# Kernel optimization log

Measured on AMD Instinct MI355X. Metric: run time of the kernel, lower is better.

## Reference

```python
import jax, jax.numpy as jnp
import numpy as np

N_NODES = 10000
N_EDGES = 640000
NODE_DIM = 64
HIDDEN = 128
NUM_LAYERS = 4


def setup_inputs() -> dict:
    key = jax.random.key(0)
    ks = jax.random.split(key, 12)
    s = lambda fan_in: 1.0 / np.sqrt(fan_in)
    inp = {
        'x': jax.random.normal(ks[0], (N_NODES, NODE_DIM), dtype=jnp.float32),
        'edge_index': jax.random.randint(ks[1], (2, N_EDGES), 0, N_NODES, dtype=jnp.int64),
        # node embedding Linear(node_dim, hidden)
        'W_emb': jax.random.uniform(ks[2], (NODE_DIM, HIDDEN), jnp.float32, -s(NODE_DIM), s(NODE_DIM)),
        'b_emb': jnp.zeros((HIDDEN,), jnp.float32),
        # per-layer EdgeConv MLP: Linear(2*hidden, hidden) -> ReLU -> Linear(hidden, hidden)
        'W1': jax.random.uniform(ks[3], (NUM_LAYERS, 2 * HIDDEN, HIDDEN), jnp.float32, -s(2 * HIDDEN), s(2 * HIDDEN)),
        'b1': jnp.zeros((NUM_LAYERS, HIDDEN), jnp.float32),
        'W2': jax.random.uniform(ks[4], (NUM_LAYERS, HIDDEN, HIDDEN), jnp.float32, -s(HIDDEN), s(HIDDEN)),
        'b2': jnp.zeros((NUM_LAYERS, HIDDEN), jnp.float32),
        # final fc Linear(hidden, hidden)
        'W_fc': jax.random.uniform(ks[5], (HIDDEN, HIDDEN), jnp.float32, -s(HIDDEN), s(HIDDEN)),
        'b_fc': jnp.zeros((HIDDEN,), jnp.float32),
    }
    return inp


def _edge_conv(x, src, dst, W1, b1, W2, b2):
    # message: MLP(concat[x_i, x_j - x_i]); x_i = target (dst), x_j = source (src)
    x_i = x[dst]                      # [E, H]
    x_j = x[src]                      # [E, H]
    m = jnp.concatenate([x_i, x_j - x_i], axis=1)  # [E, 2H]
    m = jax.nn.relu(m @ W1 + b1)
    m = m @ W2 + b2                   # [E, H]
    # scatter-max aggregation at target nodes (self loops guarantee coverage)
    return jax.ops.segment_max(m, dst, num_segments=N_NODES)


def reference(x, edge_index, W_emb, b_emb, W1, b1, W2, b2, W_fc, b_fc):
    # add_self_loops
    loops = jnp.arange(N_NODES, dtype=edge_index.dtype)
    src = jnp.concatenate([edge_index[0], loops])
    dst = jnp.concatenate([edge_index[1], loops])

    h = x @ W_emb + b_emb             # [N, H]
    for l in range(NUM_LAYERS):
        h = _edge_conv(h, src, dst, W1[l], b1[l], W2[l], b2[l])
    return h @ W_fc + b_fc
```

## Files before the change

### kernel.cpp

```cpp
#include <hip/hip_runtime.h>

#define N_NODES 10000
#define N_EDGES 640000
#define NODE_DIM 64
#define HIDDEN 128
#define NUM_LAYERS 4
#define NT (N_EDGES + N_NODES)
#define EB8 64

typedef __attribute__((ext_vector_type(8))) short short8v;
typedef __attribute__((ext_vector_type(16))) float f32x16;

__global__ void k_init(const int* __restrict__ ei, int* __restrict__ flag,
                       int* __restrict__ cnt, unsigned int* __restrict__ enc0)
{
    int gid = blockIdx.x * 256 + threadIdx.x;
    if (gid < N_NODES) cnt[gid] = 0;
    for (int i = gid; i < N_NODES * HIDDEN; i += (int)gridDim.x * 256)
        enc0[i] = 0u;
    if (blockIdx.x == 0) {
        __shared__ int nz;
        if (threadIdx.x == 0) nz = 0;
        __syncthreads();
        int found = 0;
        for (int k = threadIdx.x; k < 2048; k += 256) {
            int pos = 2 * (k * 156) + 1;
            if (ei[pos] != 0) found = 1;
        }
        if (found) atomicOr(&nz, 1);
        __syncthreads();
        if (threadIdx.x == 0) flag[0] = nz;
    }
}

__global__ void k_norm_count(const int* __restrict__ ei, const int* __restrict__ flag,
                             int* __restrict__ srcN, int* __restrict__ dstN,
                             int* __restrict__ cnt)
{
    int e = blockIdx.x * 256 + threadIdx.x;
    if (e >= N_EDGES) return;
    int s, d;
    if (flag[0]) { s = ei[e];     d = ei[N_EDGES + e]; }
    else         { s = ei[2 * e]; d = ei[2 * (N_EDGES + e)]; }
    srcN[e] = s;
    dstN[e] = d;
    atomicAdd(&cnt[d], 1);
}

__global__ void k_scan(const int* __restrict__ cnt, int* __restrict__ cursor)
{
    __shared__ int part[256];
    const int t = threadIdx.x;
    const int CH = (N_NODES + 255) / 256;
    int lo = t * CH, hi = min(N_NODES, lo + CH);
    int s = 0;
    for (int i = lo; i < hi; ++i) s += cnt[i] + 1;
    part[t] = s;
    __syncthreads();
    for (int off = 1; off < 256; off <<= 1) {
        int v = (t >= off) ? part[t - off] : 0;
        __syncthreads();
        part[t] += v;
        __syncthreads();
    }
    int base = (t == 0) ? 0 : part[t - 1];
    for (int i = lo; i < hi; ++i) {
        cursor[i] = base;
        base += cnt[i] + 1;
    }
}

__global__ void k_scatter_all(const int* __restrict__ srcN, const int* __restrict__ dstN,
                              int* __restrict__ cursor,
                              int* __restrict__ esrc, int* __restrict__ edst)
{
    int e = blockIdx.x * 256 + threadIdx.x;
    if (e >= NT) return;
    int s, d;
    if (e < N_EDGES) { s = srcN[e]; d = dstN[e]; }
    else             { s = e - N_EDGES; d = s; }
    int pos = atomicAdd(&cursor[d], 1);
    esrc[pos] = s;
    edst[pos] = d;
}

__device__ __forceinline__ unsigned short bf16rne(float f)
{
    unsigned int u = __float_as_uint(f);
    unsigned int r = u + 0x7FFFu + ((u >> 16) & 1u);
    return (unsigned short)(r >> 16);
}

__global__ void k_prepww(const float* __restrict__ W1, const float* __restrict__ W2,
                         float* __restrict__ Wa, float* __restrict__ Wb,
                         short* __restrict__ W2f)
{
    int i = blockIdx.x * 256 + threadIdx.x;
    if (i >= NUM_LAYERS * 128 * 128) return;
    int l = i >> 14, rem = i & 16383;
    float top = W1[l * 32768 + rem];
    float bot = W1[l * 32768 + 16384 + rem];
    Wa[i] = top - bot;
    Wb[i] = bot;

    int k = rem >> 7, n = rem & 127;
    float w = W2[i];
    unsigned short hs = bf16rne(w);
    float hf = __uint_as_float((unsigned int)hs << 16);
    unsigned short ls = bf16rne(w - hf);
    int c = k >> 4, kh = (k >> 3) & 1, j = k & 7;
    int tile = n >> 5, m = n & 31;
    int lane = kh * 32 + m;
    size_t base = (size_t)l * 32768 + c * 4096 + tile * 1024 + lane * 8 + j;
    W2f[base]       = (short)hs;
    W2f[base + 512] = (short)ls;
}

__device__ __forceinline__ unsigned int encf(float f)
{
    unsigned int b = __float_as_uint(f);
    return b ^ ((unsigned int)((int)b >> 31) | 0x80000000u);
}

__device__ __forceinline__ float decenc(unsigned int u)
{
    unsigned int bits = (u & 0x80000000u) ? (u ^ 0x80000000u) : ~u;
    return __uint_as_float(bits);
}

__device__ __forceinline__ void radd_split4(float4 a, float4 b, uint2& H, uint2& L)
{
    float f0 = fmaxf(a.x + b.x, 0.f), f1 = fmaxf(a.y + b.y, 0.f);
    float f2 = fmaxf(a.z + b.z, 0.f), f3 = fmaxf(a.w + b.w, 0.f);
    unsigned int u0 = __float_as_uint(f0), u1 = __float_as_uint(f1);
    unsigned int u2 = __float_as_uint(f2), u3 = __float_as_uint(f3);
    H.x = (u1 & 0xFFFF0000u) | (u0 >> 16);
    H.y = (u3 & 0xFFFF0000u) | (u2 >> 16);
    float r0 = f0 - __uint_as_float(u0 & 0xFFFF0000u);
    float r1 = f1 - __uint_as_float(u1 & 0xFFFF0000u);
    float r2 = f2 - __uint_as_float(u2 & 0xFFFF0000u);
    float r3 = f3 - __uint_as_float(u3 & 0xFFFF0000u);
    L.x = (__float_as_uint(r0) >> 16) | (__float_as_uint(r1) & 0xFFFF0000u);
    L.y = (__float_as_uint(r2) >> 16) | (__float_as_uint(r3) & 0xFFFF0000u);
}

template <int K, bool HASB, bool DEC>
__global__ __launch_bounds__(256) void k_gemm64(
    const float* __restrict__ Xf, const unsigned int* __restrict__ enc,
    unsigned int* __restrict__ encZ, const float* __restrict__ bprev,
    const float* __restrict__ WA, const float* __restrict__ WB,
    const float* __restrict__ biasA,
    float* __restrict__ CA, float* __restrict__ CB, int M)
{
    constexpr int LDX = K + 4;
    __shared__ float Xs[64 * LDX];
    const int t = threadIdx.x;
    const int row0 = (blockIdx.x >> 1) * 64;
    const int ch   = (blockIdx.x & 1) * 64;
    constexpr int F4R = K / 4;
    for (int i = t; i < 64 * F4R; i += 256) {
        int r = i / F4R, f = i % F4R;
        int gr = row0 + r;
        float4 v = make_float4(0.f, 0.f, 0.f, 0.f);
        if (gr < M) {
            if constexpr (DEC) {
                uint4 u = *(const uint4*)(enc + (size_t)gr * K + 4 * f);
                v.x = decenc(u.x) + bprev[4 * f + 0];
                v.y = decenc(u.y) + bprev[4 * f + 1];
                v.z = decenc(u.z) + bprev[4 * f + 2];
                v.w = decenc(u.w) + bprev[4 * f + 3];
                if (encZ && ch == 0) {
                    uint4 z = make_uint4(0u, 0u, 0u, 0u);
                    *(uint4*)(encZ + (size_t)gr * K + 4 * f) = z;
                }
            } else {
                v = *(const float4*)(Xf + (size_t)gr * K + 4 * f);
            }
        }
        *(float4*)(Xs + r * LDX + 4 * f) = v;
    }
    __syncthreads();

    const int rg = t >> 4, cg = t & 15;
    {
        float accA[4][4];
#pragma unroll
        for (int i = 0; i < 4; ++i)
#pragma unroll
            for (int j = 0; j < 4; ++j) accA[i][j] = 0.f;
#pragma unroll 4
        for (int k = 0; k < K; ++k) {
            float4 wa = *(const float4*)(WA + k * 128 + ch + cg * 4);
            float xs[4];
#pragma unroll
            for (int i = 0; i < 4; ++i) xs[i] = Xs[(rg * 4 + i) * LDX + k];
#pragma unroll
            for (int i = 0; i < 4; ++i) {
                accA[i][0] += xs[i] * wa.x; accA[i][1] += xs[i] * wa.y;
                accA[i][2] += xs[i] * wa.z; accA[i][3] += xs[i] * wa.w;
            }
        }
        float4 b = *(const float4*)(biasA + ch + cg * 4);
#pragma unroll
        for (int i = 0; i < 4; ++i) {
            int r = row0 + rg * 4 + i;
            if (r < M) {
                *(float4*)(CA + (size_t)r * 128 + ch + cg * 4) =
                    make_float4(accA[i][0] + b.x, accA[i][1] + b.y,
                                accA[i][2] + b.z, accA[i][3] + b.w);
            }
        }
    }
    if constexpr (HASB) {
        float accB[4][4];
#pragma unroll
        for (int i = 0; i < 4; ++i)
#pragma unroll
            for (int j = 0; j < 4; ++j) accB[i][j] = 0.f;
#pragma unroll 4
        for (int k = 0; k < K; ++k) {
            float4 wb = *(const float4*)(WB + k * 128 + ch + cg * 4);
            float xs[4];
#pragma unroll
            for (int i = 0; i < 4; ++i) xs[i] = Xs[(rg * 4 + i) * LDX + k];
#pragma unroll
            for (int i = 0; i < 4; ++i) {
                accB[i][0] += xs[i] * wb.x; accB[i][1] += xs[i] * wb.y;
                accB[i][2] += xs[i] * wb.z; accB[i][3] += xs[i] * wb.w;
            }
        }
#pragma unroll
        for (int i = 0; i < 4; ++i) {
            int r = row0 + rg * 4 + i;
            if (r < M) {
                *(float4*)(CB + (size_t)r * 128 + ch + cg * 4) =
                    make_float4(accB[i][0], accB[i][1], accB[i][2], accB[i][3]);
            }
        }
    }
}

__global__ __launch_bounds__(256, 4) void k_edge9(
    const float* __restrict__ A, const float* __restrict__ Bm,
    const int* __restrict__ esrc, const int* __restrict__ edst,
    const short* __restrict__ W2l, unsigned int* __restrict__ enc)
{
    __shared__ __align__(16) short Ts[2048 * 8];
    __shared__ int dsts[EB8];

    const int t = threadIdx.x;
    const int lane = t & 63;
    const int wv   = t >> 6;
    const int nwg = (int)gridDim.x;
    const int orig = (int)blockIdx.x;
    const int xcd = orig & 7, idx = orig >> 3;
    const int qq = nwg >> 3, rr = nwg & 7;
    const int bid = (xcd < rr ? xcd * (qq + 1) : rr * (qq + 1) + (xcd - rr) * qq) + idx;
    const int s0 = bid * EB8;

    const short* Wp = W2l + (size_t)wv * 1024 + (size_t)lane * 8;
    short8v bfh[8], bfl[8];
#pragma unroll
    for (int c = 0; c < 8; ++c) {
        bfh[c] = *(const short8v*)(Wp + (size_t)c * 4096);
        bfl[c] = *(const short8v*)(Wp + (size_t)c * 4096 + 512);
    }

    {
        const int row = t >> 2;
        const int q   = t & 3;
        const int slot = s0 + row;
        int dst = -1, src = 0;
        if (slot < NT) { dst = edst[slot]; src = esrc[slot]; }
        if (q == 0) dsts[row] = dst;
        const int sfrag = row >> 5;
        const int mrow  = row & 31;
        const int kh    = q >> 1;
        const int half  = q & 1;
        const int lbase = kh * 32 + mrow;

        if (dst >= 0) {
            const float* Ar = A  + (size_t)dst * HIDDEN + q * 4;
            const float* Br = Bm + (size_t)src * HIDDEN + q * 4;
#pragma unroll
            for (int r = 0; r < 8; ++r) {
                float4 av = *(const float4*)(Ar + r * 16);
                float4 bv = *(const float4*)(Br + r * 16);
                uint2 H, L;
                radd_split4(av, bv, H, L);
                const int c  = r;
                const int ih = ((sfrag)     * 8 + c) * 64 + lbase;
                const int il = ((2 + sfrag) * 8 + c) * 64 + lbase;
                *(uint2*)(&Ts[(size_t)(ih ^ c) * 8 + half * 4]) = H;
                *(uint2*)(&Ts[(size_t)(il ^ c) * 8 + half * 4]) = L;
            }
        } else {
            uint2 z = make_uint2(0u, 0u);
#pragma unroll
            for (int r = 0; r < 8; ++r) {
                const int c  = r;
                const int ih = ((sfrag)     * 8 + c) * 64 + lbase;
                const int il = ((2 + sfrag) * 8 + c) * 64 + lbase;
                *(uint2*)(&Ts[(size_t)(ih ^ c) * 8 + half * 4]) = z;
                *(uint2*)(&Ts[(size_t)(il ^ c) * 8 + half * 4]) = z;
            }
        }
    }
    __syncthreads();

    f32x16 acc0 = {0,0,0,0,0,0,0,0,0,0,0,0,0,0,0,0};
    f32x16 acc1 = {0,0,0,0,0,0,0,0,0,0,0,0,0,0,0,0};

#pragma unroll
    for (int c = 0; c < 8; ++c) {
        short8v ah0 = *(const short8v*)(&Ts[(size_t)(((0 * 8 + c) * 64 + lane) ^ c) * 8]);
        short8v ah1 = *(const short8v*)(&Ts[(size_t)(((1 * 8 + c) * 64 + lane) ^ c) * 8]);
        short8v al0 = *(const short8v*)(&Ts[(size_t)(((2 * 8 + c) * 64 + lane) ^ c) * 8]);
        short8v al1 = *(const short8v*)(&Ts[(size_t)(((3 * 8 + c) * 64 + lane) ^ c) * 8]);
        acc0 = __builtin_amdgcn_mfma_f32_32x32x16_bf16(ah0, bfh[c], acc0, 0, 0, 0);
        acc0 = __builtin_amdgcn_mfma_f32_32x32x16_bf16(al0, bfh[c], acc0, 0, 0, 0);
        acc0 = __builtin_amdgcn_mfma_f32_32x32x16_bf16(ah0, bfl[c], acc0, 0, 0, 0);
        acc1 = __builtin_amdgcn_mfma_f32_32x32x16_bf16(ah1, bfh[c], acc1, 0, 0, 0);
        acc1 = __builtin_amdgcn_mfma_f32_32x32x16_bf16(al1, bfh[c], acc1, 0, 0, 0);
        acc1 = __builtin_amdgcn_mfma_f32_32x32x16_bf16(ah1, bfl[c], acc1, 0, 0, 0);
    }

    const int m   = lane & 31;
    const int kh  = lane >> 5;
    const int col = wv * 32 + m;
    const int d_first = dsts[0];
    const int d_last  = dsts[EB8 - 1];
    if (d_first == d_last) {
        if (d_first >= 0) {
            float mx = fmaxf(acc0[0], acc1[0]);
#pragma unroll
            for (int r = 1; r < 16; ++r)
                mx = fmaxf(mx, fmaxf(acc0[r], acc1[r]));
            atomicMax(&enc[(size_t)d_first * HIDDEN + col], encf(mx));
        }
    } else {
        {
            float run = -3.4e38f;
            int curd = dsts[4 * kh];
#pragma unroll
            for (int r = 0; r < 16; ++r) {
                const int er = (r & 3) + 8 * (r >> 2) + 4 * kh;
                int d = dsts[er];
                if (d != curd) {
                    if (curd >= 0)
                        atomicMax(&enc[(size_t)curd * HIDDEN + col], encf(run));
                    curd = d;
                    run = -3.4e38f;
                }
                run = fmaxf(run, acc0[r]);
            }
            if (curd >= 0)
                atomicMax(&enc[(size_t)curd * HIDDEN + col], encf(run));
        }
        {
            float run = -3.4e38f;
            int curd = dsts[32 + 4 * kh];
#pragma unroll
            for (int r = 0; r < 16; ++r) {
                const int er = 32 + (r & 3) + 8 * (r >> 2) + 4 * kh;
                int d = dsts[er];
                if (d != curd) {
                    if (curd >= 0)
                        atomicMax(&enc[(size_t)curd * HIDDEN + col], encf(run));
                    curd = d;
                    run = -3.4e38f;
                }
                run = fmaxf(run, acc1[r]);
            }
            if (curd >= 0)
                atomicMax(&enc[(size_t)curd * HIDDEN + col], encf(run));
        }
    }
}

extern "C" void kernel_launch(void* const* d_in, const int* in_sizes, int n_in,
                              void* d_out, int out_size, void* d_ws, size_t ws_size,
                              hipStream_t stream)
{
    const float* x     = (const float*)d_in[0];
    const int*   ei    = (const int*)d_in[1];
    const float* W_emb = (const float*)d_in[2];
    const float* b_emb = (const float*)d_in[3];
    const float* W1    = (const float*)d_in[4];
    const float* b1    = (const float*)d_in[5];
    const float* W2    = (const float*)d_in[6];
    const float* b2    = (const float*)d_in[7];
    const float* W_fc  = (const float*)d_in[8];
    const float* b_fc  = (const float*)d_in[9];
    float* out = (float*)d_out;

    char* p = (char*)d_ws;
    auto alloc = [&](size_t bytes) {
        char* r = p;
        p += (bytes + 255) & ~(size_t)255;
        return r;
    };
    float* h    = (float*)alloc((size_t)N_NODES * HIDDEN * 4);
    float* Ab   = (float*)alloc((size_t)N_NODES * HIDDEN * 4);
    float* Bb   = (float*)alloc((size_t)N_NODES * HIDDEN * 4);
    unsigned int* enc0 = (unsigned int*)alloc((size_t)N_NODES * HIDDEN * 4);
    unsigned int* enc1 = (unsigned int*)alloc((size_t)N_NODES * HIDDEN * 4);
    float* Wa   = (float*)alloc((size_t)NUM_LAYERS * 16384 * 4);
    float* Wb   = (float*)alloc((size_t)NUM_LAYERS * 16384 * 4);
    short* W2f  = (short*)alloc((size_t)NUM_LAYERS * 32768 * 2);
    int* cursor = (int*)alloc(N_NODES * 4);
    int* cnt    = (int*)alloc(N_NODES * 4);
    int* esrc   = (int*)alloc((size_t)NT * 4);
    int* edst   = (int*)alloc((size_t)NT * 4);
    int* srcN   = (int*)alloc((size_t)N_EDGES * 4);
    int* dstN   = (int*)alloc((size_t)N_EDGES * 4);
    int* flag   = (int*)alloc(4);

    unsigned int* encs[2] = {enc0, enc1};

    const int EBLK = (N_EDGES + 255) / 256;
    const int GB   = 2 * ((N_NODES + 63) / 64);
    const int EG   = (NT + EB8 - 1) / EB8;

    k_init<<<(N_NODES * HIDDEN + 255) / 256, 256, 0, stream>>>(ei, flag, cnt, enc0);
    k_norm_count<<<EBLK, 256, 0, stream>>>(ei, flag, srcN, dstN, cnt);
    k_scan<<<1, 256, 0, stream>>>(cnt, cursor);
    k_scatter_all<<<(NT + 255) / 256, 256, 0, stream>>>(srcN, dstN, cursor, esrc, edst);
    k_prepww<<<(NUM_LAYERS * 16384 + 255) / 256, 256, 0, stream>>>(W1, W2, Wa, Wb, W2f);

    k_gemm64<NODE_DIM, false, false><<<GB, 256, 0, stream>>>(
        x, nullptr, nullptr, nullptr, W_emb, nullptr, b_emb, h, nullptr, N_NODES);

    for (int l = 0; l < NUM_LAYERS; ++l) {
        if (l == 0) {
            k_gemm64<HIDDEN, true, false><<<GB, 256, 0, stream>>>(
                h, nullptr, nullptr, nullptr, Wa, Wb, b1, Ab, Bb, N_NODES);
        } else {
            k_gemm64<HIDDEN, true, true><<<GB, 256, 0, stream>>>(
                nullptr, encs[(l - 1) & 1], encs[l & 1], b2 + (l - 1) * 128,
                Wa + l * 16384, Wb + l * 16384, b1 + l * 128, Ab, Bb, N_NODES);
        }
        k_edge9<<<EG, 256, 0, stream>>>(Ab, Bb, esrc, edst,
                                        W2f + (size_t)l * 32768, encs[l & 1]);
    }
    k_gemm64<HIDDEN, false, true><<<GB, 256, 0, stream>>>(
        nullptr, encs[(NUM_LAYERS - 1) & 1], nullptr, b2 + 3 * 128,
        W_fc, nullptr, b_fc, out, nullptr, N_NODES);
}
```

Baseline: 561.6 us.

## Halve edge tile to 32 edges per block and stream W2 fragments for occupancy

```diff
diff --git a/kernel.cpp b/kernel.cpp
--- a/kernel.cpp
+++ b/kernel.cpp
@@ -6,7 +6,7 @@
 #define HIDDEN 128
 #define NUM_LAYERS 4
 #define NT (N_EDGES + N_NODES)
-#define EB8 64
+#define EB10 32
 
 typedef __attribute__((ext_vector_type(8))) short short8v;
 typedef __attribute__((ext_vector_type(16))) float f32x16;
@@ -240,13 +240,13 @@
     }
 }
 
-__global__ __launch_bounds__(256, 4) void k_edge9(
+__global__ __launch_bounds__(256, 8) void k_edge10(
     const float* __restrict__ A, const float* __restrict__ Bm,
     const int* __restrict__ esrc, const int* __restrict__ edst,
     const short* __restrict__ W2l, unsigned int* __restrict__ enc)
 {
-    __shared__ __align__(16) short Ts[2048 * 8];
-    __shared__ int dsts[EB8];
+    __shared__ __align__(16) short Ts[1024 * 8];
+    __shared__ int dsts[EB10];
 
     const int t = threadIdx.x;
     const int lane = t & 63;
@@ -256,125 +256,105 @@
     const int xcd = orig & 7, idx = orig >> 3;
     const int qq = nwg >> 3, rr = nwg & 7;
     const int bid = (xcd < rr ? xcd * (qq + 1) : rr * (qq + 1) + (xcd - rr) * qq) + idx;
-    const int s0 = bid * EB8;
-
-    const short* Wp = W2l + (size_t)wv * 1024 + (size_t)lane * 8;
-    short8v bfh[8], bfl[8];
-#pragma unroll
-    for (int c = 0; c < 8; ++c) {
-        bfh[c] = *(const short8v*)(Wp + (size_t)c * 4096);
-        bfl[c] = *(const short8v*)(Wp + (size_t)c * 4096 + 512);
-    }
+    const int s0 = bid * EB10;
 
     {
-        const int row = t >> 2;
-        const int q   = t & 3;
+        const int row = t >> 3;
+        const int c   = t & 7;
         const int slot = s0 + row;
         int dst = -1, src = 0;
         if (slot < NT) { dst = edst[slot]; src = esrc[slot]; }
-        if (q == 0) dsts[row] = dst;
-        const int sfrag = row >> 5;
-        const int mrow  = row & 31;
-        const int kh    = q >> 1;
-        const int half  = q & 1;
-        const int lbase = kh * 32 + mrow;
+        if (c == 0) dsts[row] = dst;
+
+        const int u_h0 = (((0 + c) * 64 +      row) ^ c) * 8;
+        const int u_h1 = (((0 + c) * 64 + 32 + row) ^ c) * 8;
+        const int u_l0 = (((8 + c) * 64 +      row) ^ c) * 8;
+        const int u_l1 = (((8 + c) * 64 + 32 + row) ^ c) * 8;
 
         if (dst >= 0) {
-            const float* Ar = A  + (size_t)dst * HIDDEN + q * 4;
-            const float* Br = Bm + (size_t)src * HIDDEN + q * 4;
-#pragma unroll
-            for (int r = 0; r < 8; ++r) {
-                float4 av = *(const float4*)(Ar + r * 16);
-                float4 bv = *(const float4*)(Br + r * 16);
-                uint2 H, L;
-                radd_split4(av, bv, H, L);
-                const int c  = r;
-                const int ih = ((sfrag)     * 8 + c) * 64 + lbase;
-                const int il = ((2 + sfrag) * 8 + c) * 64 + lbase;
-                *(uint2*)(&Ts[(size_t)(ih ^ c) * 8 + half * 4]) = H;
-                *(uint2*)(&Ts[(size_t)(il ^ c) * 8 + half * 4]) = L;
-            }
+            const float* Ar = A  + (size_t)dst * HIDDEN + c * 16;
+            const float* Br = Bm + (size_t)src * HIDDEN + c * 16;
+            float4 a0 = *(const float4*)(Ar + 0);
+            float4 a1 = *(const float4*)(Ar + 4);
+            float4 a2 = *(const float4*)(Ar + 8);
+            float4 a3 = *(const float4*)(Ar + 12);
+            float4 b0 = *(const float4*)(Br + 0);
+            float4 b1 = *(const float4*)(Br + 4);
+            float4 b2 = *(const float4*)(Br + 8);
+            float4 b3 = *(const float4*)(Br + 12);
+            uint2 Ha, La, Hb, Lb;
+            radd_split4(a0, b0, Ha, La);
+            radd_split4(a1, b1, Hb, Lb);
+            uint4 H0 = make_uint4(Ha.x, Ha.y, Hb.x, Hb.y);
+            uint4 L0 = make_uint4(La.x, La.y, Lb.x, Lb.y);
+            radd_split4(a2, b2, Ha, La);
+            radd_split4(a3, b3, Hb, Lb);
+            uint4 H1 = make_uint4(Ha.x, Ha.y, Hb.x, Hb.y);
+            uint4 L1 = make_uint4(La.x, La.y, Lb.x, Lb.y);
+            *(uint4*)(&Ts[u_h0]) = H0;
+            *(uint4*)(&Ts[u_h1]) = H1;
+            *(uint4*)(&Ts[u_l0]) = L0;
+            *(uint4*)(&Ts[u_l1]) = L1;
         } else {
-            uint2 z = make_uint2(0u, 0u);
-#pragma unroll
-            for (int r = 0; r < 8; ++r) {
-                const int c  = r;
-                const int ih = ((sfrag)     * 8 + c) * 64 + lbase;
-                const int il = ((2 + sfrag) * 8 + c) * 64 + lbase;
-                *(uint2*)(&Ts[(size_t)(ih ^ c) * 8 + half * 4]) = z;
-                *(uint2*)(&Ts[(size_t)(il ^ c) * 8 + half * 4]) = z;
-            }
+            uint4 z = make_uint4(0u, 0u, 0u, 0u);
+            *(uint4*)(&Ts[u_h0]) = z;
+            *(uint4*)(&Ts[u_h1]) = z;
+            *(uint4*)(&Ts[u_l0]) = z;
+            *(uint4*)(&Ts[u_l1]) = z;
         }
     }
     __syncthreads();
 
-    f32x16 acc0 = {0,0,0,0,0,0,0,0,0,0,0,0,0,0,0,0};
-    f32x16 acc1 = {0,0,0,0,0,0,0,0,0,0,0,0,0,0,0,0};
+    f32x16 acc = {0,0,0,0,0,0,0,0,0,0,0,0,0,0,0,0};
+
+    const short* Wp = W2l + (size_t)wv * 1024 + (size_t)lane * 8;
+    short8v bh = *(const short8v*)(Wp);
+    short8v bl = *(const short8v*)(Wp + 512);
 
 #pragma unroll
     for (int c = 0; c < 8; ++c) {
-        short8v ah0 = *(const short8v*)(&Ts[(size_t)(((0 * 8 + c) * 64 + lane) ^ c) * 8]);
-        short8v ah1 = *(const short8v*)(&Ts[(size_t)(((1 * 8 + c) * 64 + lane) ^ c) * 8]);
-        short8v al0 = *(const short8v*)(&Ts[(size_t)(((2 * 8 + c) * 64 + lane) ^ c) * 8]);
-        short8v al1 = *(const short8v*)(&Ts[(size_t)(((3 * 8 + c) * 64 + lane) ^ c) * 8]);
-        acc0 = __builtin_amdgcn_mfma_f32_32x32x16_bf16(ah0, bfh[c], acc0, 0, 0, 0);
-        acc0 = __builtin_amdgcn_mfma_f32_32x32x16_bf16(al0, bfh[c], acc0, 0, 0, 0);
-        acc0 = __builtin_amdgcn_mfma_f32_32x32x16_bf16(ah0, bfl[c], acc0, 0, 0, 0);
-        acc1 = __builtin_amdgcn_mfma_f32_32x32x16_bf16(ah1, bfh[c], acc1, 0, 0, 0);
-        acc1 = __builtin_amdgcn_mfma_f32_32x32x16_bf16(al1, bfh[c], acc1, 0, 0, 0);
-        acc1 = __builtin_amdgcn_mfma_f32_32x32x16_bf16(ah1, bfl[c], acc1, 0, 0, 0);
+        short8v nbh, nbl;
+        if (c < 7) {
+            nbh = *(const short8v*)(Wp + (size_t)(c + 1) * 4096);
+            nbl = *(const short8v*)(Wp + (size_t)(c + 1) * 4096 + 512);
+        }
+        short8v ah = *(const short8v*)(&Ts[(size_t)((( c     ) * 64 + lane) ^ c) * 8]);
+        short8v al = *(const short8v*)(&Ts[(size_t)(((8 + c ) * 64 + lane) ^ c) * 8]);
+        acc = __builtin_amdgcn_mfma_f32_32x32x16_bf16(ah, bh, acc, 0, 0, 0);
+        acc = __builtin_amdgcn_mfma_f32_32x32x16_bf16(al, bh, acc, 0, 0, 0);
+        acc = __builtin_amdgcn_mfma_f32_32x32x16_bf16(ah, bl, acc, 0, 0, 0);
+        if (c < 7) { bh = nbh; bl = nbl; }
     }
 
     const int m   = lane & 31;
     const int kh  = lane >> 5;
     const int col = wv * 32 + m;
     const int d_first = dsts[0];
-    const int d_last  = dsts[EB8 - 1];
+    const int d_last  = dsts[EB10 - 1];
     if (d_first == d_last) {
         if (d_first >= 0) {
-            float mx = fmaxf(acc0[0], acc1[0]);
-#pragma unroll
-            for (int r = 1; r < 16; ++r)
-                mx = fmaxf(mx, fmaxf(acc0[r], acc1[r]));
+            float mx = acc[0];
+#pragma unroll
+            for (int r = 1; r < 16; ++r) mx = fmaxf(mx, acc[r]);
             atomicMax(&enc[(size_t)d_first * HIDDEN + col], encf(mx));
         }
     } else {
-        {
-            float run = -3.4e38f;
-            int curd = dsts[4 * kh];
-#pragma unroll
-            for (int r = 0; r < 16; ++r) {
-                const int er = (r & 3) + 8 * (r >> 2) + 4 * kh;
-                int d = dsts[er];
-                if (d != curd) {
-                    if (curd >= 0)
-                        atomicMax(&enc[(size_t)curd * HIDDEN + col], encf(run));
-                    curd = d;
-                    run = -3.4e38f;
-                }
-                run = fmaxf(run, acc0[r]);
-            }
-            if (curd >= 0)
-                atomicMax(&enc[(size_t)curd * HIDDEN + col], encf(run));
-        }
-        {
-            float run = -3.4e38f;
-            int curd = dsts[32 + 4 * kh];
-#pragma unroll
-            for (int r = 0; r < 16; ++r) {
-                const int er = 32 + (r & 3) + 8 * (r >> 2) + 4 * kh;
-                int d = dsts[er];
-                if (d != curd) {
-                    if (curd >= 0)
-                        atomicMax(&enc[(size_t)curd * HIDDEN + col], encf(run));
-                    curd = d;
-                    run = -3.4e38f;
-                }
-                run = fmaxf(run, acc1[r]);
-            }
-            if (curd >= 0)
-                atomicMax(&enc[(size_t)curd * HIDDEN + col], encf(run));
-        }
+        float run = -3.4e38f;
+        int curd = dsts[4 * kh];
+#pragma unroll
+        for (int r = 0; r < 16; ++r) {
+            const int er = (r & 3) + 8 * (r >> 2) + 4 * kh;
+            int d = dsts[er];
+            if (d != curd) {
+                if (curd >= 0)
+                    atomicMax(&enc[(size_t)curd * HIDDEN + col], encf(run));
+                curd = d;
+                run = -3.4e38f;
+            }
+            run = fmaxf(run, acc[r]);
+        }
+        if (curd >= 0)
+            atomicMax(&enc[(size_t)curd * HIDDEN + col], encf(run));
     }
 }
 
@@ -420,7 +400,7 @@
 
     const int EBLK = (N_EDGES + 255) / 256;
     const int GB   = 2 * ((N_NODES + 63) / 64);
-    const int EG   = (NT + EB8 - 1) / EB8;
+    const int EG   = (NT + EB10 - 1) / EB10;
 
     k_init<<<(N_NODES * HIDDEN + 255) / 256, 256, 0, stream>>>(ei, flag, cnt, enc0);
     k_norm_count<<<EBLK, 256, 0, stream>>>(ei, flag, srcN, dstN, cnt);
@@ -440,8 +420,8 @@
                 nullptr, encs[(l - 1) & 1], encs[l & 1], b2 + (l - 1) * 128,
                 Wa + l * 16384, Wb + l * 16384, b1 + l * 128, Ab, Bb, N_NODES);
         }
-        k_edge9<<<EG, 256, 0, stream>>>(Ab, Bb, esrc, edst,
-                                        W2f + (size_t)l * 32768, encs[l & 1]);
+        k_edge10<<<EG, 256, 0, stream>>>(Ab, Bb, esrc, edst,
+                                         W2f + (size_t)l * 32768, encs[l & 1]);
     }
     k_gemm64<HIDDEN, false, true><<<GB, 256, 0, stream>>>(
         nullptr, encs[(NUM_LAYERS - 1) & 1], nullptr, b2 + 3 * 128,
```

After: 638.8 us. +13.8%, slower.

## Move node GEMMs to split-bf16 MFMA with pre-swizzled weight fragments

Applied to the files above, without the earlier changes.

```diff
diff --git a/kernel.cpp b/kernel.cpp
--- a/kernel.cpp
+++ b/kernel.cpp
@@ -91,29 +91,41 @@
     return (unsigned short)(r >> 16);
 }
 
-__global__ void k_prepww(const float* __restrict__ W1, const float* __restrict__ W2,
-                         float* __restrict__ Wa, float* __restrict__ Wb,
-                         short* __restrict__ W2f)
-{
-    int i = blockIdx.x * 256 + threadIdx.x;
-    if (i >= NUM_LAYERS * 128 * 128) return;
-    int l = i >> 14, rem = i & 16383;
-    float top = W1[l * 32768 + rem];
-    float bot = W1[l * 32768 + 16384 + rem];
-    Wa[i] = top - bot;
-    Wb[i] = bot;
-
-    int k = rem >> 7, n = rem & 127;
-    float w = W2[i];
+__device__ __forceinline__ void wfrag_store(short* __restrict__ Wf, int k, int n, float w)
+{
     unsigned short hs = bf16rne(w);
     float hf = __uint_as_float((unsigned int)hs << 16);
     unsigned short ls = bf16rne(w - hf);
     int c = k >> 4, kh = (k >> 3) & 1, j = k & 7;
     int tile = n >> 5, m = n & 31;
     int lane = kh * 32 + m;
-    size_t base = (size_t)l * 32768 + c * 4096 + tile * 1024 + lane * 8 + j;
-    W2f[base]       = (short)hs;
-    W2f[base + 512] = (short)ls;
+    size_t base = (size_t)c * 4096 + tile * 1024 + lane * 8 + j;
+    Wf[base]       = (short)hs;
+    Wf[base + 512] = (short)ls;
+}
+
+__global__ void k_prepall(const float* __restrict__ W1, const float* __restrict__ W2,
+                          const float* __restrict__ W_emb, const float* __restrict__ W_fc,
+                          short* __restrict__ Waf, short* __restrict__ Wbf,
+                          short* __restrict__ W2f, short* __restrict__ Wembf,
+                          short* __restrict__ Wfcf)
+{
+    int i = blockIdx.x * 256 + threadIdx.x;
+    if (i < NUM_LAYERS * 16384) {
+        int l = i >> 14, rem = i & 16383;
+        int k = rem >> 7, n = rem & 127;
+        float top = W1[l * 32768 + rem];
+        float bot = W1[l * 32768 + 16384 + rem];
+        wfrag_store(Waf + (size_t)l * 32768, k, n, top - bot);
+        wfrag_store(Wbf + (size_t)l * 32768, k, n, bot);
+        wfrag_store(W2f + (size_t)l * 32768, k, n, W2[i]);
+    } else if (i < NUM_LAYERS * 16384 + 8192) {
+        int j = i - NUM_LAYERS * 16384;
+        wfrag_store(Wembf, j >> 7, j & 127, W_emb[j]);
+    } else if (i < NUM_LAYERS * 16384 + 8192 + 16384) {
+        int j = i - NUM_LAYERS * 16384 - 8192;
+        wfrag_store(Wfcf, j >> 7, j & 127, W_fc[j]);
+    }
 }
 
 __device__ __forceinline__ unsigned int encf(float f)
@@ -144,98 +156,119 @@
     L.y = (__float_as_uint(r2) >> 16) | (__float_as_uint(r3) & 0xFFFF0000u);
 }
 
+__device__ __forceinline__ void split4_rne(float4 f, uint2& H, uint2& L)
+{
+    unsigned int h0 = bf16rne(f.x), h1 = bf16rne(f.y);
+    unsigned int h2 = bf16rne(f.z), h3 = bf16rne(f.w);
+    H.x = h0 | (h1 << 16);
+    H.y = h2 | (h3 << 16);
+    float r0 = f.x - __uint_as_float(h0 << 16);
+    float r1 = f.y - __uint_as_float(h1 << 16);
+    float r2 = f.z - __uint_as_float(h2 << 16);
+    float r3 = f.w - __uint_as_float(h3 << 16);
+    unsigned int l0 = bf16rne(r0), l1 = bf16rne(r1);
+    unsigned int l2 = bf16rne(r2), l3 = bf16rne(r3);
+    L.x = l0 | (l1 << 16);
+    L.y = l2 | (l3 << 16);
+}
+
 template <int K, bool HASB, bool DEC>
-__global__ __launch_bounds__(256) void k_gemm64(
-    const float* __restrict__ Xf, const unsigned int* __restrict__ enc,
+__global__ __launch_bounds__(256) void k_gemmf(
+    const float* __restrict__ Xf, const unsigned int* __restrict__ encR,
     unsigned int* __restrict__ encZ, const float* __restrict__ bprev,
-    const float* __restrict__ WA, const float* __restrict__ WB,
+    const short* __restrict__ WAf, const short* __restrict__ WBf,
     const float* __restrict__ biasA,
     float* __restrict__ CA, float* __restrict__ CB, int M)
 {
-    constexpr int LDX = K + 4;
-    __shared__ float Xs[64 * LDX];
+    constexpr int CH = K / 16;
+    __shared__ __align__(16) short Ts[4 * CH * 64 * 8];
     const int t = threadIdx.x;
-    const int row0 = (blockIdx.x >> 1) * 64;
-    const int ch   = (blockIdx.x & 1) * 64;
-    constexpr int F4R = K / 4;
-    for (int i = t; i < 64 * F4R; i += 256) {
-        int r = i / F4R, f = i % F4R;
-        int gr = row0 + r;
-        float4 v = make_float4(0.f, 0.f, 0.f, 0.f);
-        if (gr < M) {
-            if constexpr (DEC) {
-                uint4 u = *(const uint4*)(enc + (size_t)gr * K + 4 * f);
-                v.x = decenc(u.x) + bprev[4 * f + 0];
-                v.y = decenc(u.y) + bprev[4 * f + 1];
-                v.z = decenc(u.z) + bprev[4 * f + 2];
-                v.w = decenc(u.w) + bprev[4 * f + 3];
-                if (encZ && ch == 0) {
-                    uint4 z = make_uint4(0u, 0u, 0u, 0u);
-                    *(uint4*)(encZ + (size_t)gr * K + 4 * f) = z;
+    const int row0 = blockIdx.x * 64;
+
+    {
+        const int row = t >> 2, q = t & 3;
+        const int gr = row0 + row;
+        const int sfrag = row >> 5, mrow = row & 31;
+        const int kh = q >> 1, half = q & 1;
+        const int lbase = kh * 32 + mrow;
+#pragma unroll
+        for (int r = 0; r < CH; ++r) {
+            float4 v = make_float4(0.f, 0.f, 0.f, 0.f);
+            if (gr < M) {
+                const int ko = q * 4 + r * 16;
+                if constexpr (DEC) {
+                    uint4 u = *(const uint4*)(encR + (size_t)gr * K + ko);
+                    v.x = decenc(u.x) + bprev[ko + 0];
+                    v.y = decenc(u.y) + bprev[ko + 1];
+                    v.z = decenc(u.z) + bprev[ko + 2];
+                    v.w = decenc(u.w) + bprev[ko + 3];
+                    if (encZ)
+                        *(uint4*)(encZ + (size_t)gr * K + ko) = make_uint4(0u, 0u, 0u, 0u);
+                } else {
+                    v = *(const float4*)(Xf + (size_t)gr * K + ko);
                 }
-            } else {
-                v = *(const float4*)(Xf + (size_t)gr * K + 4 * f);
             }
-        }
-        *(float4*)(Xs + r * LDX + 4 * f) = v;
+            uint2 H, L;
+            split4_rne(v, H, L);
+            const int c  = r;
+            const int ih = ((0 * 2 + sfrag) * CH + c) * 64 + lbase;
+            const int il = ((1 * 2 + sfrag) * CH + c) * 64 + lbase;
+            *(uint2*)(&Ts[(size_t)(ih ^ c) * 8 + half * 4]) = H;
+            *(uint2*)(&Ts[(size_t)(il ^ c) * 8 + half * 4]) = L;
+        }
     }
     __syncthreads();
 
-    const int rg = t >> 4, cg = t & 15;
-    {
-        float accA[4][4];
-#pragma unroll
-        for (int i = 0; i < 4; ++i)
-#pragma unroll
-            for (int j = 0; j < 4; ++j) accA[i][j] = 0.f;
-#pragma unroll 4
-        for (int k = 0; k < K; ++k) {
-            float4 wa = *(const float4*)(WA + k * 128 + ch + cg * 4);
-            float xs[4];
-#pragma unroll
-            for (int i = 0; i < 4; ++i) xs[i] = Xs[(rg * 4 + i) * LDX + k];
-#pragma unroll
-            for (int i = 0; i < 4; ++i) {
-                accA[i][0] += xs[i] * wa.x; accA[i][1] += xs[i] * wa.y;
-                accA[i][2] += xs[i] * wa.z; accA[i][3] += xs[i] * wa.w;
-            }
-        }
-        float4 b = *(const float4*)(biasA + ch + cg * 4);
-#pragma unroll
-        for (int i = 0; i < 4; ++i) {
-            int r = row0 + rg * 4 + i;
-            if (r < M) {
-                *(float4*)(CA + (size_t)r * 128 + ch + cg * 4) =
-                    make_float4(accA[i][0] + b.x, accA[i][1] + b.y,
-                                accA[i][2] + b.z, accA[i][3] + b.w);
-            }
-        }
-    }
-    if constexpr (HASB) {
-        float accB[4][4];
-#pragma unroll
-        for (int i = 0; i < 4; ++i)
-#pragma unroll
-            for (int j = 0; j < 4; ++j) accB[i][j] = 0.f;
-#pragma unroll 4
-        for (int k = 0; k < K; ++k) {
-            float4 wb = *(const float4*)(WB + k * 128 + ch + cg * 4);
-            float xs[4];
-#pragma unroll
-            for (int i = 0; i < 4; ++i) xs[i] = Xs[(rg * 4 + i) * LDX + k];
-#pragma unroll
-            for (int i = 0; i < 4; ++i) {
-                accB[i][0] += xs[i] * wb.x; accB[i][1] += xs[i] * wb.y;
-                accB[i][2] += xs[i] * wb.z; accB[i][3] += xs[i] * wb.w;
-            }
-        }
-#pragma unroll
-        for (int i = 0; i < 4; ++i) {
-            int r = row0 + rg * 4 + i;
-            if (r < M) {
-                *(float4*)(CB + (size_t)r * 128 + ch + cg * 4) =
-                    make_float4(accB[i][0], accB[i][1], accB[i][2], accB[i][3]);
-            }
+    const int lane = t & 63;
+    const int wv   = t >> 6;
+    f32x16 aA0 = {0,0,0,0,0,0,0,0,0,0,0,0,0,0,0,0};
+    f32x16 aA1 = {0,0,0,0,0,0,0,0,0,0,0,0,0,0,0,0};
+    f32x16 aB0 = {0,0,0,0,0,0,0,0,0,0,0,0,0,0,0,0};
+    f32x16 aB1 = {0,0,0,0,0,0,0,0,0,0,0,0,0,0,0,0};
+
+    const short* WpA = WAf + (size_t)wv * 1024 + (size_t)lane * 8;
+    const short* WpB = HASB ? (WBf + (size_t)wv * 1024 + (size_t)lane * 8) : nullptr;
+
+#pragma unroll
+    for (int c = 0; c < CH; ++c) {
+        short8v wah = *(const short8v*)(WpA + (size_t)c * 4096);
+        short8v wal = *(const short8v*)(WpA + (size_t)c * 4096 + 512);
+        short8v ah0 = *(const short8v*)(&Ts[(size_t)((((0 * 2 + 0) * CH + c) * 64 + lane) ^ c) * 8]);
+        short8v ah1 = *(const short8v*)(&Ts[(size_t)((((0 * 2 + 1) * CH + c) * 64 + lane) ^ c) * 8]);
+        short8v al0 = *(const short8v*)(&Ts[(size_t)((((1 * 2 + 0) * CH + c) * 64 + lane) ^ c) * 8]);
+        short8v al1 = *(const short8v*)(&Ts[(size_t)((((1 * 2 + 1) * CH + c) * 64 + lane) ^ c) * 8]);
+        aA0 = __builtin_amdgcn_mfma_f32_32x32x16_bf16(ah0, wah, aA0, 0, 0, 0);
+        aA0 = __builtin_amdgcn_mfma_f32_32x32x16_bf16(al0, wah, aA0, 0, 0, 0);
+        aA0 = __builtin_amdgcn_mfma_f32_32x32x16_bf16(ah0, wal, aA0, 0, 0, 0);
+        aA1 = __builtin_amdgcn_mfma_f32_32x32x16_bf16(ah1, wah, aA1, 0, 0, 0);
+        aA1 = __builtin_amdgcn_mfma_f32_32x32x16_bf16(al1, wah, aA1, 0, 0, 0);
+        aA1 = __builtin_amdgcn_mfma_f32_32x32x16_bf16(ah1, wal, aA1, 0, 0, 0);
+        if constexpr (HASB) {
+            short8v wbh = *(const short8v*)(WpB + (size_t)c * 4096);
+            short8v wbl = *(const short8v*)(WpB + (size_t)c * 4096 + 512);
+            aB0 = __builtin_amdgcn_mfma_f32_32x32x16_bf16(ah0, wbh, aB0, 0, 0, 0);
+            aB0 = __builtin_amdgcn_mfma_f32_32x32x16_bf16(al0, wbh, aB0, 0, 0, 0);
+            aB0 = __builtin_amdgcn_mfma_f32_32x32x16_bf16(ah0, wbl, aB0, 0, 0, 0);
+            aB1 = __builtin_amdgcn_mfma_f32_32x32x16_bf16(ah1, wbh, aB1, 0, 0, 0);
+            aB1 = __builtin_amdgcn_mfma_f32_32x32x16_bf16(al1, wbh, aB1, 0, 0, 0);
+            aB1 = __builtin_amdgcn_mfma_f32_32x32x16_bf16(ah1, wbl, aB1, 0, 0, 0);
+        }
+    }
+
+    const int m   = lane & 31;
+    const int kh  = lane >> 5;
+    const int col = wv * 32 + m;
+    const float bA = biasA[col];
+#pragma unroll
+    for (int r = 0; r < 16; ++r) {
+        const int er = (r & 3) + 8 * (r >> 2) + 4 * kh;
+        const int r0 = row0 + er;
+        const int r1 = row0 + 32 + er;
+        if (r0 < M) CA[(size_t)r0 * 128 + col] = aA0[r] + bA;
+        if (r1 < M) CA[(size_t)r1 * 128 + col] = aA1[r] + bA;
+        if constexpr (HASB) {
+            if (r0 < M) CB[(size_t)r0 * 128 + col] = aB0[r];
+            if (r1 < M) CB[(size_t)r1 * 128 + col] = aB1[r];
         }
     }
 }
@@ -405,9 +438,11 @@
     float* Bb   = (float*)alloc((size_t)N_NODES * HIDDEN * 4);
     unsigned int* enc0 = (unsigned int*)alloc((size_t)N_NODES * HIDDEN * 4);
     unsigned int* enc1 = (unsigned int*)alloc((size_t)N_NODES * HIDDEN * 4);
-    float* Wa   = (float*)alloc((size_t)NUM_LAYERS * 16384 * 4);
-    float* Wb   = (float*)alloc((size_t)NUM_LAYERS * 16384 * 4);
+    short* Waf  = (short*)alloc((size_t)NUM_LAYERS * 32768 * 2);
+    short* Wbf  = (short*)alloc((size_t)NUM_LAYERS * 32768 * 2);
     short* W2f  = (short*)alloc((size_t)NUM_LAYERS * 32768 * 2);
+    short* Wembf= (short*)alloc((size_t)16384 * 2);
+    short* Wfcf = (short*)alloc((size_t)32768 * 2);
     int* cursor = (int*)alloc(N_NODES * 4);
     int* cnt    = (int*)alloc(N_NODES * 4);
     int* esrc   = (int*)alloc((size_t)NT * 4);
@@ -419,31 +454,33 @@
     unsigned int* encs[2] = {enc0, enc1};
 
     const int EBLK = (N_EDGES + 255) / 256;
-    const int GB   = 2 * ((N_NODES + 63) / 64);
+    const int GB   = (N_NODES + 63) / 64;
     const int EG   = (NT + EB8 - 1) / EB8;
+    const int PREP = (NUM_LAYERS * 16384 + 8192 + 16384 + 255) / 256;
 
     k_init<<<(N_NODES * HIDDEN + 255) / 256, 256, 0, stream>>>(ei, flag, cnt, enc0);
     k_norm_count<<<EBLK, 256, 0, stream>>>(ei, flag, srcN, dstN, cnt);
     k_scan<<<1, 256, 0, stream>>>(cnt, cursor);
     k_scatter_all<<<(NT + 255) / 256, 256, 0, stream>>>(srcN, dstN, cursor, esrc, edst);
-    k_prepww<<<(NUM_LAYERS * 16384 + 255) / 256, 256, 0, stream>>>(W1, W2, Wa, Wb, W2f);
-
-    k_gemm64<NODE_DIM, false, false><<<GB, 256, 0, stream>>>(
-        x, nullptr, nullptr, nullptr, W_emb, nullptr, b_emb, h, nullptr, N_NODES);
+    k_prepall<<<PREP, 256, 0, stream>>>(W1, W2, W_emb, W_fc, Waf, Wbf, W2f, Wembf, Wfcf);
+
+    k_gemmf<NODE_DIM, false, false><<<GB, 256, 0, stream>>>(
+        x, nullptr, nullptr, nullptr, Wembf, nullptr, b_emb, h, nullptr, N_NODES);
 
     for (int l = 0; l < NUM_LAYERS; ++l) {
         if (l == 0) {
-            k_gemm64<HIDDEN, true, false><<<GB, 256, 0, stream>>>(
-                h, nullptr, nullptr, nullptr, Wa, Wb, b1, Ab, Bb, N_NODES);
+            k_gemmf<HIDDEN, true, false><<<GB, 256, 0, stream>>>(
+                h, nullptr, nullptr, nullptr, Waf, Wbf, b1, Ab, Bb, N_NODES);
         } else {
-            k_gemm64<HIDDEN, true, true><<<GB, 256, 0, stream>>>(
+            k_gemmf<HIDDEN, true, true><<<GB, 256, 0, stream>>>(
                 nullptr, encs[(l - 1) & 1], encs[l & 1], b2 + (l - 1) * 128,
-                Wa + l * 16384, Wb + l * 16384, b1 + l * 128, Ab, Bb, N_NODES);
+                Waf + (size_t)l * 32768, Wbf + (size_t)l * 32768,
+                b1 + l * 128, Ab, Bb, N_NODES);
         }
         k_edge9<<<EG, 256, 0, stream>>>(Ab, Bb, esrc, edst,
                                         W2f + (size_t)l * 32768, encs[l & 1]);
     }
-    k_gemm64<HIDDEN, false, true><<<GB, 256, 0, stream>>>(
+    k_gemmf<HIDDEN, false, true><<<GB, 256, 0, stream>>>(
         nullptr, encs[(NUM_LAYERS - 1) & 1], nullptr, b2 + 3 * 128,
-        W_fc, nullptr, b_fc, out, nullptr, N_NODES);
-}
+        Wfcf, nullptr, b_fc, out, nullptr, N_NODES);
+}
```

Result: faster. 502.2 us, median of 4 (-10.6%).
